# Kernel tuning notes

Hardware: AMD Instinct MI355X
Metric: run time of the kernel (lower is better)

The kernel has to match this reference:

```python
import jax, jax.numpy as jnp
import numpy as np

BATCH, DIM = 32, 512
STDDEV = 0.1


def _annihilation(dim):
    # diag(sqrt(1..dim-1), k=1), complex64
    d = jnp.sqrt(jnp.arange(1, dim, dtype=jnp.float32)).astype(jnp.complex64)
    return jnp.diag(d, k=1)


def setup_inputs() -> dict:
    key = jax.random.key(0)
    ks = jax.random.split(key, 8)
    f = lambda k, shape: jax.random.normal(k, shape, dtype=jnp.float32)
    return {
        'inputs_re': f(ks[0], (BATCH, DIM, DIM)),
        'inputs_im': f(ks[1], (BATCH, DIM, DIM)),
        'theta_1': f(ks[2], (1,)) * STDDEV,
        'theta_2': f(ks[3], (1,)) * STDDEV,
        'r': f(ks[4], (1,)) * STDDEV,
        'bx': f(ks[5], (1,)) * STDDEV,
        'bp': f(ks[6], (1,)) * STDDEV,
        'kappa': f(ks[7], (1,)) * STDDEV,
    }


def _forward(inputs_re, inputs_im, theta_1, theta_2, r, bx, bp, kappa):
    dim = inputs_re.shape[-1]
    x = jax.lax.complex(inputs_re, inputs_im)  # [B, dim, dim] complex64

    a = _annihilation(dim)                     # [dim, dim]
    a_dag = a.conj().T
    n_diag = jnp.arange(dim, dtype=jnp.float32).astype(jnp.complex64)  # number-operator diagonal

    # Rotation operators: expm(-1i*theta*N) with N diagonal -> closed-form diagonal exp (same math)
    th1 = theta_1[0].astype(jnp.complex64)
    th2 = theta_2[0].astype(jnp.complex64)
    R1 = jnp.diag(jnp.exp(-1j * th1 * n_diag))
    R2 = jnp.diag(jnp.exp(-1j * th2 * n_diag))

    # Kerr operator: expm(1i*kappa * (N*N elementwise)) ; N diagonal so N*N = diag(k^2)
    kap = kappa[0].astype(jnp.complex64)
    K = jnp.diag(jnp.exp(1j * kap * n_diag * n_diag))

    # Squeezing: in the TF source, '*' is ELEMENTWISE, and adjoint(a) (subdiag) elementwise
    # times a (superdiag) is the zero matrix -> generator is identically 0 -> S = expm(0) = I.
    # We keep the (zero) generator in the graph so r stays a (zero-grad) primal.
    r_c = r[0].astype(jnp.complex64)
    M_S = 0.5 * (r_c * (a_dag * a) - jnp.conj(r_c) * (a * a_dag))  # exactly zeros
    S = jnp.eye(dim, dtype=jnp.complex64) + M_S

    # Displacement: D = expm(alpha*a_dag - conj(alpha)*a). Generator M is skew-Hermitian,
    # so M = iH with H = -iM Hermitian; D = V diag(exp(i*w)) V^H via eigh (exact, differentiable).
    alpha = jax.lax.complex(bx[0], bp[0])
    M = alpha * a_dag - jnp.conj(alpha) * a
    H = (-1j) * M
    w, V = jnp.linalg.eigh(H)  # w real [dim], V [dim, dim]
    D = (V * jnp.exp(1j * w.astype(jnp.complex64))[None, :]) @ V.conj().T

    # Apply gates in the original order; operators are per-sample identical so
    # broadcast one [dim,dim] matrix over the batch instead of tiling.
    y = jnp.einsum('ij,bjk->bik', R1, x)
    y = jnp.einsum('ij,bjk->bik', S, y)
    y = jnp.einsum('ij,bjk->bik', R2, y)
    y = jnp.einsum('ij,bjk->bik', D, y)
    y = jnp.einsum('ij,bjk->bik', K, y)
    return y


def reference(inputs_re, inputs_im, theta_1, theta_2, r, bx, bp, kappa):
    return _forward(inputs_re, inputs_im, theta_1, theta_2, r, bx, bp, kappa)
```

## Files before the change

kernel.cpp:

```cpp
#include <hip/hip_runtime.h>
#include <hip/hip_fp16.h>

#define DIM 512
#define BATCH 32

typedef _Float16 half8 __attribute__((ext_vector_type(8)));
typedef float floatx4 __attribute__((ext_vector_type(4)));

static __device__ __forceinline__ unsigned short f2h(float f) {
    __half h = __float2half(f);
    return *reinterpret_cast<unsigned short*>(&h);
}

__global__ __launch_bounds__(256) void taylor_tables(const float* __restrict__ bxp,
                                                     const float* __restrict__ bpp,
                                                     const float* __restrict__ th1p,
                                                     const float* __restrict__ th2p,
                                                     const float* __restrict__ kapp,
                                                     float2* __restrict__ E,
                                                     float2* __restrict__ pm,
                                                     float2* __restrict__ pj) {
    if (blockIdx.x == 128) {
        for (int u = threadIdx.x; u < 2 * DIM; u += 256) {
            if (u < DIM) {
                float s, c;
                sincosf(kapp[0] * (float)(u * u), &s, &c);
                pm[u] = make_float2(c, s);
            } else {
                const int j = u - DIM;
                float s, c;
                sincosf(-(th1p[0] + th2p[0]) * (float)j, &s, &c);
                pj[j] = make_float2(c, s);
            }
        }
        return;
    }

    const int wave = (blockIdx.x * blockDim.x + threadIdx.x) >> 6;
    const int lane = threadIdx.x & 63;
    if (wave >= DIM) return;
    const int i = wave;
    const float bx = bxp[0], bp = bpp[0];
    const float invs = 0.5f;
    const int o = lane - 31;
    const int j = i + o;
    const bool jvalid = (j >= 0 && j < DIM);

    float pre = 0.f, pim = 0.f;
    if (o == -1 && i >= 1)      { float g = sqrtf((float)i)       * invs; pre =  bx * g; pim = bp * g; }
    if (o ==  1 && i + 1 < DIM) { float g = sqrtf((float)(i + 1)) * invs; pre = -bx * g; pim = bp * g; }
    float ere = (o == 0 ? 1.f : 0.f) + pre;
    float eim = pim;

    const float gs = (jvalid && j >= 1)       ? sqrtf((float)j)       * invs : 0.f;
    const float hs = (jvalid && j + 1 < DIM)  ? sqrtf((float)(j + 1)) * invs : 0.f;
    const float csup_re = -bx * gs, csup_im = bp * gs;
    const float csub_re =  bx * hs, csub_im = bp * hs;

    for (int k = 2; k <= 30; ++k) {
        const float invk = 1.f / (float)k;
        float pmre = __shfl_up(pre, 1, 64),   pmim = __shfl_up(pim, 1, 64);
        float ppre = __shfl_down(pre, 1, 64), ppim = __shfl_down(pim, 1, 64);
        if (lane == 0)  { pmre = 0.f; pmim = 0.f; }
        if (lane == 63) { ppre = 0.f; ppim = 0.f; }
        float nre = pmre * csup_re - pmim * csup_im + ppre * csub_re - ppim * csub_im;
        float nim = pmre * csup_im + pmim * csup_re + ppre * csub_im + ppim * csub_re;
        pre = nre * invk; pim = nim * invk;
        ere += pre; eim += pim;
    }

    for (int base = 0; base < DIM; base += 64) {
        const int c = base + lane;
        const int src = c - i + 31;
        const float tre = __shfl(ere, src & 63, 64);
        const float tim = __shfl(eim, src & 63, 64);
        float vre = 0.f, vim = 0.f;
        if (src >= 0 && src < 64) { vre = tre; vim = tim; }
        E[i * DIM + c] = make_float2(vre, vim);
    }
}

__global__ __launch_bounds__(256) void csq_fold32(const float2* __restrict__ A,
                                                  unsigned short* __restrict__ Gp,
                                                  const float2* __restrict__ pm,
                                                  const float2* __restrict__ pj) {
    __shared__ float2 At[16][33];
    __shared__ float2 Bt[16][33];
    const int j0 = blockIdx.x * 32, i0 = blockIdx.y * 32;
    const int tid = threadIdx.x;
    const int tx = tid & 15, ty = tid >> 4;
    const int lmin = max(0, max(i0, j0) - 32);
    const int lmax = min(DIM, min(i0, j0) + 64);

    float cre[2][2] = {{0.f}}, cim[2][2] = {{0.f}};
    for (int lt = lmin; lt < lmax; lt += 16) {
        for (int idx = tid; idx < 512; idx += 256) {
            const int r = idx >> 4, c = idx & 15;
            const int l = lt + c;
            At[c][r] = (l < lmax) ? A[(i0 + r) * DIM + l]       : make_float2(0.f, 0.f);
            Bt[c][r] = (l < lmax) ? A[(size_t)l * DIM + j0 + r] : make_float2(0.f, 0.f);
        }
        __syncthreads();
#pragma unroll
        for (int ll = 0; ll < 16; ++ll) {
            float2 a0 = At[ll][ty * 2], a1 = At[ll][ty * 2 + 1];
            float2 b0 = Bt[ll][tx * 2], b1 = Bt[ll][tx * 2 + 1];
            cre[0][0] += a0.x * b0.x - a0.y * b0.y;  cim[0][0] += a0.x * b0.y + a0.y * b0.x;
            cre[0][1] += a0.x * b1.x - a0.y * b1.y;  cim[0][1] += a0.x * b1.y + a0.y * b1.x;
            cre[1][0] += a1.x * b0.x - a1.y * b0.y;  cim[1][0] += a1.x * b0.y + a1.y * b0.x;
            cre[1][1] += a1.x * b1.x - a1.y * b1.y;  cim[1][1] += a1.x * b1.y + a1.y * b1.x;
        }
        __syncthreads();
    }

#pragma unroll
    for (int q = 0; q < 2; ++q) {
        const int m = i0 + ty * 2 + q;
        const float2 km = pm[m];
#pragma unroll
        for (int r = 0; r < 2; ++r) {
            const int j = j0 + tx * 2 + r;
            const float2 tj = pj[j];
            const float r1 = cre[q][r] * tj.x - cim[q][r] * tj.y;
            const float i1 = cre[q][r] * tj.y + cim[q][r] * tj.x;
            const float r2 = r1 * km.x - i1 * km.y;
            const float i2 = r1 * km.y + i1 * km.x;
            *reinterpret_cast<ushort2*>(Gp + (size_t)m * 1024 + 2 * j) =
                make_ushort2(f2h(r2), f2h(-i2));
        }
    }
}

__global__ __launch_bounds__(64, 4) void apply_fused(const unsigned short* __restrict__ Gp,
                                                     const float* __restrict__ xre,
                                                     const float* __restrict__ xim,
                                                     float* __restrict__ out) {
    const int orig = blockIdx.x;
    const int wgid = (orig & 7) * 512 + (orig >> 3);
    const int b   = wgid >> 7;
    const int rem = wgid & 127;
    const int m0  = (rem >> 4) * 64;
    const int k0  = (rem & 15) * 32;

    const int lane = threadIdx.x;
    const int lr = lane & 15;
    const int lq = lane >> 4;
    const int lk8 = lq * 8;

    const int jmin = max(0, m0 - 64);
    const int jmax = min(DIM, m0 + 128);
    const int nchunk = (jmax - jmin) >> 5;

    const size_t xbase = ((size_t)b * DIM + jmin + lq * 4) * DIM + k0 + lr;
    const unsigned short* gp = Gp + (size_t)(m0 + lr) * 1024 + 2 * jmin + lk8;

    floatx4 acc[4][2];
#pragma unroll
    for (int ms = 0; ms < 4; ++ms)
#pragma unroll
        for (int ns = 0; ns < 2; ++ns) {
            acc[ms][ns][0] = 0.f; acc[ms][ns][1] = 0.f;
            acc[ms][ns][2] = 0.f; acc[ms][ns][3] = 0.f;
        }

    float rr[2][2][4], ri[2][2][4];
    half8 hb[2][2];

#define LOADRAW(CH)                                                              \
    {                                                                            \
        _Pragma("unroll")                                                        \
        for (int s = 0; s < 2; ++s)                                              \
            _Pragma("unroll")                                                    \
            for (int ns = 0; ns < 2; ++ns)                                       \
                _Pragma("unroll")                                                \
                for (int jj = 0; jj < 4; ++jj) {                                 \
                    const size_t o = xbase + (size_t)((CH) * 32 + s * 16 + jj) * DIM + ns * 16; \
                    rr[s][ns][jj] = xre[o];                                      \
                    ri[s][ns][jj] = xim[o];                                      \
                }                                                                \
    }

#define CVT()                                                                    \
    {                                                                            \
        _Pragma("unroll")                                                        \
        for (int s = 0; s < 2; ++s)                                              \
            _Pragma("unroll")                                                    \
            for (int ns = 0; ns < 2; ++ns) {                                     \
                union { half8 h; ushort2 u2[4]; } u;                             \
                _Pragma("unroll")                                                \
                for (int jj = 0; jj < 4; ++jj)                                   \
                    u.u2[jj] = make_ushort2(f2h(rr[s][ns][jj]), f2h(ri[s][ns][jj])); \
                hb[s][ns] = u.h;                                                 \
            }                                                                    \
    }

#define MFMA_CHUNK(CH)                                                           \
    {                                                                            \
        __builtin_amdgcn_s_setprio(1);                                           \
        _Pragma("unroll")                                                        \
        for (int s = 0; s < 2; ++s) {                                            \
            half8 a[4];                                                          \
            _Pragma("unroll")                                                    \
            for (int ms = 0; ms < 4; ++ms)                                       \
                a[ms] = *reinterpret_cast<const half8*>(gp + (size_t)ms * 16 * 1024 + (CH) * 64 + s * 32); \
            _Pragma("unroll")                                                    \
            for (int ms = 0; ms < 4; ++ms)                                       \
                _Pragma("unroll")                                                \
                for (int ns = 0; ns < 2; ++ns)                                   \
                    acc[ms][ns] = __builtin_amdgcn_mfma_f32_16x16x32_f16(a[ms], hb[s][ns], acc[ms][ns], 0, 0, 0); \
        }                                                                        \
        __builtin_amdgcn_s_setprio(0);                                           \
    }

    LOADRAW(0);
    for (int ch = 0; ch < nchunk; ++ch) {
        CVT();
        if (ch + 1 < nchunk) LOADRAW(ch + 1);
        MFMA_CHUNK(ch);
    }

    const int crow = lq * 4;
#pragma unroll
    for (int ms = 0; ms < 4; ++ms) {
#pragma unroll
        for (int ns = 0; ns < 2; ++ns) {
            const int kk = k0 + ns * 16 + lr;
#pragma unroll
            for (int e = 0; e < 4; ++e) {
                const int m = m0 + ms * 16 + crow + e;
                out[((size_t)b * DIM + m) * DIM + kk] = acc[ms][ns][e];
            }
        }
    }
#undef LOADRAW
#undef CVT
#undef MFMA_CHUNK
}

extern "C" void kernel_launch(void* const* d_in, const int* in_sizes, int n_in,
                              void* d_out, int out_size, void* d_ws, size_t ws_size,
                              hipStream_t stream) {
    const float* xre = (const float*)d_in[0];
    const float* xim = (const float*)d_in[1];
    const float* th1 = (const float*)d_in[2];
    const float* th2 = (const float*)d_in[3];
    const float* bx  = (const float*)d_in[5];
    const float* bp  = (const float*)d_in[6];
    const float* kap = (const float*)d_in[7];
    float* out = (float*)d_out;

    char* ws = (char*)d_ws;
    float2* E           = (float2*)ws;
    unsigned short* Gp  = (unsigned short*)(ws + 2u * 1024 * 1024);
    float2* pm          = (float2*)(ws + 3u * 1024 * 1024);
    float2* pj          = pm + DIM;

    hipLaunchKernelGGL(taylor_tables, dim3(129), dim3(256), 0, stream,
                       bx, bp, th1, th2, kap, E, pm, pj);
    hipLaunchKernelGGL(csq_fold32, dim3(16, 16), dim3(256), 0, stream,
                       E, Gp, pm, pj);
    hipLaunchKernelGGL(apply_fused, dim3(4096), dim3(64), 0, stream,
                       Gp, xre, xim, out);
}
```

Before: 60.59 us.

## Double-buffer x loads two chunks ahead and use nontemporal output stores

```diff
diff --git a/kernel.cpp b/kernel.cpp
--- a/kernel.cpp
+++ b/kernel.cpp
@@ -131,7 +131,7 @@
     }
 }
 
-__global__ __launch_bounds__(64, 4) void apply_fused(const unsigned short* __restrict__ Gp,
+__global__ __launch_bounds__(64, 3) void apply_fused(const unsigned short* __restrict__ Gp,
                                                      const float* __restrict__ xre,
                                                      const float* __restrict__ xim,
                                                      float* __restrict__ out) {
@@ -163,10 +163,11 @@
             acc[ms][ns][2] = 0.f; acc[ms][ns][3] = 0.f;
         }
 
-    float rr[2][2][4], ri[2][2][4];
+    float xrA[2][2][4], xiA[2][2][4], xrB[2][2][4], xiB[2][2][4];
+    half8 ha[2][4];
     half8 hb[2][2];
 
-#define LOADRAW(CH)                                                              \
+#define LOADX(RR, RI, CH)                                                        \
     {                                                                            \
         _Pragma("unroll")                                                        \
         for (int s = 0; s < 2; ++s)                                              \
@@ -175,12 +176,21 @@
                 _Pragma("unroll")                                                \
                 for (int jj = 0; jj < 4; ++jj) {                                 \
                     const size_t o = xbase + (size_t)((CH) * 32 + s * 16 + jj) * DIM + ns * 16; \
-                    rr[s][ns][jj] = xre[o];                                      \
-                    ri[s][ns][jj] = xim[o];                                      \
+                    RR[s][ns][jj] = xre[o];                                      \
+                    RI[s][ns][jj] = xim[o];                                      \
                 }                                                                \
     }
 
-#define CVT()                                                                    \
+#define LOADA(CH)                                                                \
+    {                                                                            \
+        _Pragma("unroll")                                                        \
+        for (int s = 0; s < 2; ++s)                                              \
+            _Pragma("unroll")                                                    \
+            for (int ms = 0; ms < 4; ++ms)                                       \
+                ha[s][ms] = *reinterpret_cast<const half8*>(gp + (size_t)ms * 16 * 1024 + (CH) * 64 + s * 32); \
+    }
+
+#define CVTX(RR, RI)                                                             \
     {                                                                            \
         _Pragma("unroll")                                                        \
         for (int s = 0; s < 2; ++s)                                              \
@@ -189,34 +199,36 @@
                 union { half8 h; ushort2 u2[4]; } u;                             \
                 _Pragma("unroll")                                                \
                 for (int jj = 0; jj < 4; ++jj)                                   \
-                    u.u2[jj] = make_ushort2(f2h(rr[s][ns][jj]), f2h(ri[s][ns][jj])); \
+                    u.u2[jj] = make_ushort2(f2h(RR[s][ns][jj]), f2h(RI[s][ns][jj])); \
                 hb[s][ns] = u.h;                                                 \
             }                                                                    \
     }
 
-#define MFMA_CHUNK(CH)                                                           \
+#define MFMA_CH()                                                                \
     {                                                                            \
         __builtin_amdgcn_s_setprio(1);                                           \
         _Pragma("unroll")                                                        \
-        for (int s = 0; s < 2; ++s) {                                            \
-            half8 a[4];                                                          \
-            _Pragma("unroll")                                                    \
-            for (int ms = 0; ms < 4; ++ms)                                       \
-                a[ms] = *reinterpret_cast<const half8*>(gp + (size_t)ms * 16 * 1024 + (CH) * 64 + s * 32); \
+        for (int s = 0; s < 2; ++s)                                              \
             _Pragma("unroll")                                                    \
             for (int ms = 0; ms < 4; ++ms)                                       \
                 _Pragma("unroll")                                                \
                 for (int ns = 0; ns < 2; ++ns)                                   \
-                    acc[ms][ns] = __builtin_amdgcn_mfma_f32_16x16x32_f16(a[ms], hb[s][ns], acc[ms][ns], 0, 0, 0); \
-        }                                                                        \
+                    acc[ms][ns] = __builtin_amdgcn_mfma_f32_16x16x32_f16(ha[s][ms], hb[s][ns], acc[ms][ns], 0, 0, 0); \
         __builtin_amdgcn_s_setprio(0);                                           \
     }
 
-    LOADRAW(0);
-    for (int ch = 0; ch < nchunk; ++ch) {
-        CVT();
-        if (ch + 1 < nchunk) LOADRAW(ch + 1);
-        MFMA_CHUNK(ch);
+    LOADX(xrA, xiA, 0);
+    LOADX(xrB, xiB, 1);
+
+    for (int ch = 0; ch < nchunk; ch += 2) {
+        LOADA(ch);
+        CVTX(xrA, xiA);
+        if (ch + 2 < nchunk) LOADX(xrA, xiA, ch + 2);
+        MFMA_CH();
+        LOADA(ch + 1);
+        CVTX(xrB, xiB);
+        if (ch + 3 < nchunk) LOADX(xrB, xiB, ch + 3);
+        MFMA_CH();
     }
 
     const int crow = lq * 4;
@@ -228,13 +240,15 @@
 #pragma unroll
             for (int e = 0; e < 4; ++e) {
                 const int m = m0 + ms * 16 + crow + e;
-                out[((size_t)b * DIM + m) * DIM + kk] = acc[ms][ns][e];
+                __builtin_nontemporal_store(acc[ms][ns][e],
+                                            out + ((size_t)b * DIM + m) * DIM + kk);
             }
         }
     }
-#undef LOADRAW
-#undef CVT
-#undef MFMA_CHUNK
+#undef LOADX
+#undef LOADA
+#undef CVTX
+#undef MFMA_CH
 }
 
 extern "C" void kernel_launch(void* const* d_in, const int* in_sizes, int n_in,
```

Result: slower. 68.02 us (+12.3%).
